# Performance work log

Hardware: AMD Instinct MI355X
Metric: run time of the kernel (lower is better)

The kernel has to match this reference:

```python
import jax, jax.numpy as jnp
import numpy as np

LEAK = 0.01  # F.leaky_relu default negative_slope


def projection(p, cam, res):
    # Weak-perspective projection to normalized [-1,1] image coords.
    # cam = [s, tx, ty]; p [B,N,3] -> [B,N,2]
    s = cam[:, 0][:, None, None]
    t = cam[:, None, 1:3]
    return s * (p[..., :2] + t)


def grid_sample_points(im_feat, pts):
    # Bilinear grid_sample with align_corners=True, zeros padding,
    # specialized to a [B,N,1,2] point grid (matches points.unsqueeze(2)).
    # im_feat [B,C,H,W], pts [B,N,2] in [-1,1] -> [B,C,N]
    B, C, H, W = im_feat.shape
    N = pts.shape[1]
    x = (pts[..., 0] + 1.0) * 0.5 * (W - 1)
    y = (pts[..., 1] + 1.0) * 0.5 * (H - 1)
    x0 = jnp.floor(x)
    y0 = jnp.floor(y)
    x1 = x0 + 1.0
    y1 = y0 + 1.0
    wx1 = x - x0
    wx0 = 1.0 - wx1
    wy1 = y - y0
    wy0 = 1.0 - wy1
    feat_flat = im_feat.reshape(B, C, H * W)

    def gather(xi, yi, w):
        valid = (xi >= 0) & (xi <= W - 1) & (yi >= 0) & (yi <= H - 1)
        xc = jnp.clip(xi, 0, W - 1).astype(jnp.int32)
        yc = jnp.clip(yi, 0, H - 1).astype(jnp.int32)
        idx = (yc * W + xc)[:, None, :]  # [B,1,N]
        g = jnp.take_along_axis(feat_flat, jnp.broadcast_to(idx, (B, C, N)), axis=2)
        return g * (w * valid.astype(w.dtype))[:, None, :]

    return (gather(x0, y0, wx0 * wy0) + gather(x1, y0, wx1 * wy0)
            + gather(x0, y1, wx0 * wy1) + gather(x1, y1, wx1 * wy1))


def reduce_dim(feat, W0, b0, W1, b1, W2, b2):
    # feat [B,C0,N]; Conv1d kernel_size=1 == channel matmul.
    def conv1x1(x, W, b):
        return jnp.einsum('oc,bcn->bon', W, x) + b[None, :, None]

    y = jax.nn.leaky_relu(conv1x1(feat, W0, b0), LEAK)
    y = jax.nn.leaky_relu(conv1x1(jnp.concatenate([y, feat], axis=1), W1, b1), LEAK)
    y = conv1x1(jnp.concatenate([y, feat], axis=1), W2, b2)
    y = jax.nn.relu(y)  # last_op
    return y.reshape(y.shape[0], -1)  # [B, C_p*N]


def setup_inputs() -> dict:
    key = jax.random.key(0)
    ks = jax.random.split(key, 9)
    B, N, C, H, Wd = 64, 431, 256, 56, 56
    dims = [256, 128, 64, 5]
    p = jax.random.normal(ks[0], (B, N, 3), jnp.float32)
    cam = jax.random.uniform(ks[1], (B, 3), jnp.float32)
    s_feat = jax.random.normal(ks[2], (B, C, H, Wd), jnp.float32)
    W0 = jax.random.normal(ks[3], (dims[1], dims[0]), jnp.float32) * 0.02
    b0 = jnp.zeros((dims[1],), jnp.float32)
    W1 = jax.random.normal(ks[4], (dims[2], dims[1] + dims[0]), jnp.float32) * 0.02
    b1 = jnp.zeros((dims[2],), jnp.float32)
    W2 = jax.random.normal(ks[5], (dims[3], dims[2] + dims[0]), jnp.float32) * 0.02
    b2 = jnp.zeros((dims[3],), jnp.float32)
    return {"p": p, "cam": cam, "s_feat": s_feat,
            "W0": W0, "b0": b0, "W1": W1, "b1": b1, "W2": W2, "b2": b2,
            "res": 224}


def reference(p, cam, s_feat, W0, b0, W1, b1, W2, b2, res):
    p2d = projection(p, cam, res)                 # [B,N,2]
    point_feat = grid_sample_points(s_feat, p2d)  # [B,C_s,N]
    return reduce_dim(point_feat, W0, b0, W1, b1, W2, b2)  # [B, C_p*N]
```

## Files before the change

### kernel.cpp

```cpp
#include <hip/hip_runtime.h>


#define B_   64
#define N_   431
#define C_   256
#define H_   56
#define W_   56
#define HW_  3136
#define PPB  16
#define NT_  27
#define NPAD (NT_ * PPB)

#define Y0S  136
#define Y1S  72

typedef __attribute__((ext_vector_type(8))) short short8;
typedef __attribute__((ext_vector_type(4))) float f32x4;

__device__ __forceinline__ ushort f2bf(float f) {
    unsigned u = __float_as_uint(f);
    u += 0x7fffu + ((u >> 16) & 1u);
    return (ushort)(u >> 16);
}
__device__ __forceinline__ uint pack2(float lo, float hi) {
    return (uint)f2bf(lo) | ((uint)f2bf(hi) << 16);
}
__device__ __forceinline__ float lo16(uint u) { return __uint_as_float(u << 16); }
__device__ __forceinline__ float hi16(uint u) { return __uint_as_float(u & 0xffff0000u); }

#define WTOT (128 * 256 + 64 * 384 + 16 * 320)
#define GB_  (B_ * 64)

__global__ __launch_bounds__(256, 6) void gather_kernel(
    const float* __restrict__ p,
    const float* __restrict__ cam,
    const float* __restrict__ sfeat,
    const float* __restrict__ W0,
    const float* __restrict__ W1,
    const float* __restrict__ W2,
    ushort* __restrict__ feat,
    ushort* __restrict__ W0b,
    ushort* __restrict__ W1b,
    ushort* __restrict__ W2p)
{
    const int bx = blockIdx.x;
    if (bx >= GB_) {
        const int t0 = (bx - GB_) * 256 + threadIdx.x;
        for (int i = t0; i < WTOT; i += 8 * 256) {
            if (i < 128 * 256) {
                W0b[i] = f2bf(W0[i]);
            } else if (i < 128 * 256 + 64 * 384) {
                const int j = i - 128 * 256;
                W1b[j] = f2bf(W1[j]);
            } else {
                const int j = i - (128 * 256 + 64 * 384);
                const int r = j / 320, c = j - r * 320;
                W2p[j] = (r < 5) ? f2bf(W2[r * 320 + c]) : (ushort)0;
            }
        }
        return;
    }

    __shared__ uint plane01[HW_];
    __shared__ uint plane23[HW_];

    const int b  = bx >> 6;
    const int cg = bx & 63;
    const int c0 = cg * 4;
    const int t  = threadIdx.x;

    {
        const float4* __restrict__ s0 = (const float4*)(sfeat + ((size_t)b * C_ + c0 + 0) * HW_);
        const float4* __restrict__ s1 = (const float4*)(sfeat + ((size_t)b * C_ + c0 + 1) * HW_);
        const float4* __restrict__ s2 = (const float4*)(sfeat + ((size_t)b * C_ + c0 + 2) * HW_);
        const float4* __restrict__ s3 = (const float4*)(sfeat + ((size_t)b * C_ + c0 + 3) * HW_);
        for (int k = t; k < HW_ / 4; k += 256) {
            const float4 a = s0[k], bb = s1[k];
            uint4 u01;
            u01.x = pack2(a.x, bb.x); u01.y = pack2(a.y, bb.y);
            u01.z = pack2(a.z, bb.z); u01.w = pack2(a.w, bb.w);
            *(uint4*)&plane01[k * 4] = u01;
            const float4 c = s2[k], d = s3[k];
            uint4 u23;
            u23.x = pack2(c.x, d.x); u23.y = pack2(c.y, d.y);
            u23.z = pack2(c.z, d.z); u23.w = pack2(c.w, d.w);
            *(uint4*)&plane23[k * 4] = u23;
        }
    }
    __syncthreads();

    const float s  = cam[b * 3 + 0];
    const float tx = cam[b * 3 + 1];
    const float ty = cam[b * 3 + 2];
    ushort* __restrict__ fdst = feat + ((size_t)b * 64 + cg) * NPAD * 4;

    for (int n = t; n < NPAD; n += 256) {
        int   i00 = 0, i10 = 0, i01 = 0, i11 = 0;
        float w00 = 0.f, w10 = 0.f, w01 = 0.f, w11 = 0.f;
        if (n < N_) {
            const float px = p[((size_t)b * N_ + n) * 3 + 0];
            const float py = p[((size_t)b * N_ + n) * 3 + 1];
            const float x = (s * (px + tx) + 1.f) * 0.5f * (float)(W_ - 1);
            const float y = (s * (py + ty) + 1.f) * 0.5f * (float)(H_ - 1);
            const float x0f = floorf(x), y0f = floorf(y);
            const float wx1 = x - x0f, wx0 = 1.f - wx1;
            const float wy1 = y - y0f, wy0 = 1.f - wy1;
            const int ix0 = (int)x0f, iy0 = (int)y0f;
            const int ix1 = ix0 + 1,  iy1 = iy0 + 1;
            const bool vx0 = (ix0 >= 0) & (ix0 <= W_ - 1);
            const bool vx1 = (ix1 >= 0) & (ix1 <= W_ - 1);
            const bool vy0 = (iy0 >= 0) & (iy0 <= H_ - 1);
            const bool vy1 = (iy1 >= 0) & (iy1 <= H_ - 1);
            const int cx0 = min(max(ix0, 0), W_ - 1);
            const int cx1 = min(max(ix1, 0), W_ - 1);
            const int cy0 = min(max(iy0, 0), H_ - 1);
            const int cy1 = min(max(iy1, 0), H_ - 1);
            w00 = (vx0 & vy0) ? wx0 * wy0 : 0.f;
            w10 = (vx1 & vy0) ? wx1 * wy0 : 0.f;
            w01 = (vx0 & vy1) ? wx0 * wy1 : 0.f;
            w11 = (vx1 & vy1) ? wx1 * wy1 : 0.f;
            i00 = cy0 * W_ + cx0;  i10 = cy0 * W_ + cx1;
            i01 = cy1 * W_ + cx0;  i11 = cy1 * W_ + cx1;
        }
        const uint a00 = plane01[i00], a10 = plane01[i10], a01 = plane01[i01], a11 = plane01[i11];
        const uint c00 = plane23[i00], c10 = plane23[i10], c01 = plane23[i01], c11 = plane23[i11];
        const float v0 = w00 * lo16(a00) + w10 * lo16(a10) + w01 * lo16(a01) + w11 * lo16(a11);
        const float v1 = w00 * hi16(a00) + w10 * hi16(a10) + w01 * hi16(a01) + w11 * hi16(a11);
        const float v2 = w00 * lo16(c00) + w10 * lo16(c10) + w01 * lo16(c01) + w11 * lo16(c11);
        const float v3 = w00 * hi16(c00) + w10 * hi16(c10) + w01 * hi16(c01) + w11 * hi16(c11);
        ushort4 r;
        r.x = f2bf(v0); r.y = f2bf(v1); r.z = f2bf(v2); r.w = f2bf(v3);
        *(ushort4*)(fdst + (size_t)n * 4) = r;
    }
}

__global__ __launch_bounds__(256, 4) void mlp_kernel(
    const ushort* __restrict__ feat,
    const ushort* __restrict__ W0b,
    const float* __restrict__ b0,
    const ushort* __restrict__ W1b,
    const float* __restrict__ b1,
    const ushort* __restrict__ W2p,
    const float* __restrict__ b2,
    float* __restrict__ out)
{
    __shared__ ushort y0_s[PPB * Y0S];
    __shared__ ushort y1_s[PPB * Y1S];

    const int tid  = threadIdx.x;
    const int w    = tid >> 6;
    const int l    = tid & 63;
    const int m    = l & 15;
    const int q    = l >> 4;
    const int tile = blockIdx.x;
    const int b    = blockIdx.y;
    const int n0   = tile * PPB;
    const int n    = n0 + m;

    const ushort* __restrict__ fb = feat + (size_t)b * 64 * NPAD * 4;
    short8 af[8];
    #pragma unroll
    for (int ks = 0; ks < 8; ++ks) {
        const int cg0 = 8 * ks + 2 * q;
        union { short8 v; uint2 u[2]; } tmp;
        tmp.u[0] = *(const uint2*)(fb + ((size_t)cg0 * NPAD + n) * 4);
        tmp.u[1] = *(const uint2*)(fb + ((size_t)(cg0 + 1) * NPAD + n) * 4);
        af[ks] = tmp.v;
    }

    {
        f32x4 acc0 = {0.f, 0.f, 0.f, 0.f};
        f32x4 acc1 = {0.f, 0.f, 0.f, 0.f};
        const ushort* __restrict__ wr0 = W0b + ((size_t)(2 * w) * 16 + m) * 256 + 8 * q;
        const ushort* __restrict__ wr1 = wr0 + 16 * 256;
        #pragma unroll
        for (int ks = 0; ks < 8; ++ks) {
            const short8 w0 = *(const short8*)(wr0 + 32 * ks);
            const short8 w1 = *(const short8*)(wr1 + 32 * ks);
            acc0 = __builtin_amdgcn_mfma_f32_16x16x32_bf16(af[ks], w0, acc0, 0, 0, 0);
            acc1 = __builtin_amdgcn_mfma_f32_16x16x32_bf16(af[ks], w1, acc1, 0, 0, 0);
        }
        const int o0 = (2 * w) * 16 + m, o1 = o0 + 16;
        const float bias0 = b0[o0], bias1 = b0[o1];
        #pragma unroll
        for (int r = 0; r < 4; ++r) {
            float v0 = acc0[r] + bias0; v0 = (v0 > 0.f) ? v0 : 0.01f * v0;
            float v1 = acc1[r] + bias1; v1 = (v1 > 0.f) ? v1 : 0.01f * v1;
            y0_s[(q * 4 + r) * Y0S + o0] = f2bf(v0);
            y0_s[(q * 4 + r) * Y0S + o1] = f2bf(v1);
        }
    }
    __syncthreads();

    {
        f32x4 acc = {0.f, 0.f, 0.f, 0.f};
        const ushort* __restrict__ wr = W1b + ((size_t)w * 16 + m) * 384 + 8 * q;
        #pragma unroll
        for (int ks = 0; ks < 4; ++ks) {
            const short8 a  = *(const short8*)(y0_s + m * Y0S + 32 * ks + 8 * q);
            const short8 bb = *(const short8*)(wr + 32 * ks);
            acc = __builtin_amdgcn_mfma_f32_16x16x32_bf16(a, bb, acc, 0, 0, 0);
        }
        #pragma unroll
        for (int ks = 4; ks < 12; ++ks) {
            const short8 bb = *(const short8*)(wr + 32 * ks);
            acc = __builtin_amdgcn_mfma_f32_16x16x32_bf16(af[ks - 4], bb, acc, 0, 0, 0);
        }
        const int o = w * 16 + m;
        const float bias = b1[o];
        #pragma unroll
        for (int r = 0; r < 4; ++r) {
            float v = acc[r] + bias; v = (v > 0.f) ? v : 0.01f * v;
            y1_s[(q * 4 + r) * Y1S + o] = f2bf(v);
        }
    }
    __syncthreads();

    if (w == 0) {
        f32x4 acc = {0.f, 0.f, 0.f, 0.f};
        const ushort* __restrict__ wr = W2p + (size_t)m * 320 + 8 * q;
        #pragma unroll
        for (int ks = 0; ks < 2; ++ks) {
            const short8 a  = *(const short8*)(y1_s + m * Y1S + 32 * ks + 8 * q);
            const short8 bb = *(const short8*)(wr + 32 * ks);
            acc = __builtin_amdgcn_mfma_f32_16x16x32_bf16(a, bb, acc, 0, 0, 0);
        }
        #pragma unroll
        for (int ks = 2; ks < 10; ++ks) {
            const short8 bb = *(const short8*)(wr + 32 * ks);
            acc = __builtin_amdgcn_mfma_f32_16x16x32_bf16(af[ks - 2], bb, acc, 0, 0, 0);
        }
        if (m < 5) {
            const float bias = b2[m];
            #pragma unroll
            for (int r = 0; r < 4; ++r) {
                const int nn = n0 + q * 4 + r;
                if (nn < N_) {
                    float v = acc[r] + bias;
                    out[((size_t)b * 5 + m) * N_ + nn] = (v > 0.f) ? v : 0.f;
                }
            }
        }
    }
}

__global__ __launch_bounds__(256, 4) void maf_fallback_kernel(
    const float* __restrict__ p, const float* __restrict__ cam,
    const float* __restrict__ sfeat,
    const float* __restrict__ W0, const float* __restrict__ b0,
    const float* __restrict__ W1, const float* __restrict__ b1,
    const float* __restrict__ W2, const float* __restrict__ b2,
    float* __restrict__ out)
{
    __shared__ float feat_s[PPB][C_ + 4];
    __shared__ float y0_s[PPB][128 + 4];
    __shared__ float y1_s[PPB][64 + 4];

    const int tid = threadIdx.x;
    const int b   = blockIdx.y;
    const int n0  = blockIdx.x * PPB;
    const float s  = cam[b * 3 + 0];
    const float tx = cam[b * 3 + 1];
    const float ty = cam[b * 3 + 2];
    {
        const int c = tid;
        const float* __restrict__ fb = sfeat + ((size_t)b * C_ + c) * HW_;
        for (int pp = 0; pp < PPB; ++pp) {
            const int n = n0 + pp;
            float val = 0.f;
            if (n < N_) {
                const float px = p[((size_t)b * N_ + n) * 3 + 0];
                const float py = p[((size_t)b * N_ + n) * 3 + 1];
                const float x = (s * (px + tx) + 1.f) * 0.5f * (float)(W_ - 1);
                const float y = (s * (py + ty) + 1.f) * 0.5f * (float)(H_ - 1);
                const float x0f = floorf(x), y0f = floorf(y);
                const float wx1 = x - x0f, wx0 = 1.f - wx1;
                const float wy1 = y - y0f, wy0 = 1.f - wy1;
                const int ix0 = (int)x0f, iy0 = (int)y0f;
                const int ix1 = ix0 + 1,  iy1 = iy0 + 1;
                const bool vx0 = (ix0 >= 0) & (ix0 <= W_ - 1);
                const bool vx1 = (ix1 >= 0) & (ix1 <= W_ - 1);
                const bool vy0 = (iy0 >= 0) & (iy0 <= H_ - 1);
                const bool vy1 = (iy1 >= 0) & (iy1 <= H_ - 1);
                const int cx0 = min(max(ix0, 0), W_ - 1);
                const int cx1 = min(max(ix1, 0), W_ - 1);
                const int cy0 = min(max(iy0, 0), H_ - 1);
                const int cy1 = min(max(iy1, 0), H_ - 1);
                const float w00 = (vx0 & vy0) ? wx0 * wy0 : 0.f;
                const float w10 = (vx1 & vy0) ? wx1 * wy0 : 0.f;
                const float w01 = (vx0 & vy1) ? wx0 * wy1 : 0.f;
                const float w11 = (vx1 & vy1) ? wx1 * wy1 : 0.f;
                val = w00 * fb[cy0 * W_ + cx0] + w10 * fb[cy0 * W_ + cx1]
                    + w01 * fb[cy1 * W_ + cx0] + w11 * fb[cy1 * W_ + cx1];
            }
            feat_s[pp][c] = val;
        }
    }
    __syncthreads();
    {
        const int o = tid & 127, pg = tid >> 7, p0 = pg * 8;
        const float* __restrict__ wr = W0 + (size_t)o * 256;
        float acc[8] = {0, 0, 0, 0, 0, 0, 0, 0};
        for (int k = 0; k < 256; k += 4) {
            const float4 w = *(const float4*)(wr + k);
            for (int i = 0; i < 8; ++i) {
                const float4 f = *(const float4*)&feat_s[p0 + i][k];
                acc[i] += w.x * f.x + w.y * f.y + w.z * f.z + w.w * f.w;
            }
        }
        const float bias = b0[o];
        for (int i = 0; i < 8; ++i) {
            const float v = acc[i] + bias;
            y0_s[p0 + i][o] = (v > 0.f) ? v : 0.01f * v;
        }
    }
    __syncthreads();
    {
        const int o = tid & 63, pg = tid >> 6, p0 = pg * 4;
        const float* __restrict__ wr = W1 + (size_t)o * 384;
        float acc[4] = {0, 0, 0, 0};
        for (int k = 0; k < 128; k += 4) {
            const float4 w = *(const float4*)(wr + k);
            for (int i = 0; i < 4; ++i) {
                const float4 f = *(const float4*)&y0_s[p0 + i][k];
                acc[i] += w.x * f.x + w.y * f.y + w.z * f.z + w.w * f.w;
            }
        }
        for (int k = 0; k < 256; k += 4) {
            const float4 w = *(const float4*)(wr + 128 + k);
            for (int i = 0; i < 4; ++i) {
                const float4 f = *(const float4*)&feat_s[p0 + i][k];
                acc[i] += w.x * f.x + w.y * f.y + w.z * f.z + w.w * f.w;
            }
        }
        const float bias = b1[o];
        for (int i = 0; i < 4; ++i) {
            const float v = acc[i] + bias;
            y1_s[p0 + i][o] = (v > 0.f) ? v : 0.01f * v;
        }
    }
    __syncthreads();
    if (tid < 80) {
        const int o = tid >> 4, pp = tid & 15;
        const float* __restrict__ wr = W2 + (size_t)o * 320;
        float acc = 0.f;
        for (int k = 0; k < 64; k += 4) {
            const float4 w = *(const float4*)(wr + k);
            const float4 f = *(const float4*)&y1_s[pp][k];
            acc += w.x * f.x + w.y * f.y + w.z * f.z + w.w * f.w;
        }
        for (int k = 0; k < 256; k += 4) {
            const float4 w = *(const float4*)(wr + 64 + k);
            const float4 f = *(const float4*)&feat_s[pp][k];
            acc += w.x * f.x + w.y * f.y + w.z * f.z + w.w * f.w;
        }
        const int n = n0 + pp;
        if (n < N_) {
            float v = acc + b2[o];
            out[((size_t)b * 5 + o) * N_ + n] = (v > 0.f) ? v : 0.f;
        }
    }
}

extern "C" void kernel_launch(void* const* d_in, const int* in_sizes, int n_in,
                              void* d_out, int out_size, void* d_ws, size_t ws_size,
                              hipStream_t stream) {
    const float* p     = (const float*)d_in[0];
    const float* cam   = (const float*)d_in[1];
    const float* sfeat = (const float*)d_in[2];
    const float* W0    = (const float*)d_in[3];
    const float* b0    = (const float*)d_in[4];
    const float* W1    = (const float*)d_in[5];
    const float* b1    = (const float*)d_in[6];
    const float* W2    = (const float*)d_in[7];
    const float* b2    = (const float*)d_in[8];
    float* out = (float*)d_out;

    const size_t feat_elems = (size_t)B_ * 64 * NPAD * 4;
    size_t off = feat_elems;
    const size_t w0_off = off; off += 128 * 256;
    const size_t w1_off = off; off += 64 * 384;
    const size_t w2_off = off; off += 16 * 320;
    const size_t need = off * sizeof(ushort);

    if (ws_size >= need) {
        ushort* feat = (ushort*)d_ws;
        ushort* W0b  = feat + w0_off;
        ushort* W1b  = feat + w1_off;
        ushort* W2p  = feat + w2_off;
        gather_kernel<<<GB_ + 8, 256, 0, stream>>>(
            p, cam, sfeat, W0, W1, W2, feat, W0b, W1b, W2p);
        mlp_kernel<<<dim3(NT_, B_), 256, 0, stream>>>(
            feat, W0b, b0, W1b, b1, W2p, b2, out);
    } else {
        maf_fallback_kernel<<<dim3(NT_, B_), 256, 0, stream>>>(
            p, cam, sfeat, W0, b0, W1, b1, W2, b2, out);
    }
}
```

Baseline: 336.7 us.

## Replace two-kernel bf16 gather+MFMA pipeline with single fused fp32 kernel

Drops the separate gather kernel, which streamed every full feature plane into LDS as bf16, and the MFMA-based MLP kernel. A single fused kernel replaces them. It first computes the bilinear indices and weights for the block's 16 points into shared memory. Each thread then gathers one channel directly from global memory, and the three 1x1 convs run in fp32 scalar FMA from LDS. This avoids reading the whole feature map and the intermediate workspace round trip, but the gathers are now scattered across channel planes (uncoalesced) and the matmuls lose tensor-core use.

After: 519.9 us. +54.4%, slower.

```diff
diff --git a/kernel.cpp b/kernel.cpp
--- a/kernel.cpp
+++ b/kernel.cpp
@@ -9,95 +9,34 @@
 #define HW_  3136
 #define PPB  16
 #define NT_  27
-#define NPAD (NT_ * PPB)
 
-#define Y0S  136
-#define Y1S  72
-
-typedef __attribute__((ext_vector_type(8))) short short8;
-typedef __attribute__((ext_vector_type(4))) float f32x4;
-
-__device__ __forceinline__ ushort f2bf(float f) {
-    unsigned u = __float_as_uint(f);
-    u += 0x7fffu + ((u >> 16) & 1u);
-    return (ushort)(u >> 16);
-}
-__device__ __forceinline__ uint pack2(float lo, float hi) {
-    return (uint)f2bf(lo) | ((uint)f2bf(hi) << 16);
-}
-__device__ __forceinline__ float lo16(uint u) { return __uint_as_float(u << 16); }
-__device__ __forceinline__ float hi16(uint u) { return __uint_as_float(u & 0xffff0000u); }
-
-#define WTOT (128 * 256 + 64 * 384 + 16 * 320)
-#define GB_  (B_ * 64)
-
-__global__ __launch_bounds__(256, 6) void gather_kernel(
+__global__ __launch_bounds__(256, 4) void maf_fused_kernel(
     const float* __restrict__ p,
     const float* __restrict__ cam,
     const float* __restrict__ sfeat,
-    const float* __restrict__ W0,
-    const float* __restrict__ W1,
-    const float* __restrict__ W2,
-    ushort* __restrict__ feat,
-    ushort* __restrict__ W0b,
-    ushort* __restrict__ W1b,
-    ushort* __restrict__ W2p)
+    const float* __restrict__ W0, const float* __restrict__ b0,
+    const float* __restrict__ W1, const float* __restrict__ b1,
+    const float* __restrict__ W2, const float* __restrict__ b2,
+    float* __restrict__ out)
 {
-    const int bx = blockIdx.x;
-    if (bx >= GB_) {
-        const int t0 = (bx - GB_) * 256 + threadIdx.x;
-        for (int i = t0; i < WTOT; i += 8 * 256) {
-            if (i < 128 * 256) {
-                W0b[i] = f2bf(W0[i]);
-            } else if (i < 128 * 256 + 64 * 384) {
-                const int j = i - 128 * 256;
-                W1b[j] = f2bf(W1[j]);
-            } else {
-                const int j = i - (128 * 256 + 64 * 384);
-                const int r = j / 320, c = j - r * 320;
-                W2p[j] = (r < 5) ? f2bf(W2[r * 320 + c]) : (ushort)0;
-            }
-        }
-        return;
-    }
+    __shared__ float feat_s[PPB][C_ + 4];
+    __shared__ float y0_s[PPB][128 + 4];
+    __shared__ float y1_s[PPB][64 + 4];
+    __shared__ int   gi_s[PPB][4];
+    __shared__ float gw_s[PPB][4];
 
-    __shared__ uint plane01[HW_];
-    __shared__ uint plane23[HW_];
+    const int tid = threadIdx.x;
+    const int b   = blockIdx.y;
+    const int n0  = blockIdx.x * PPB;
 
-    const int b  = bx >> 6;
-    const int cg = bx & 63;
-    const int c0 = cg * 4;
-    const int t  = threadIdx.x;
-
-    {
-        const float4* __restrict__ s0 = (const float4*)(sfeat + ((size_t)b * C_ + c0 + 0) * HW_);
-        const float4* __restrict__ s1 = (const float4*)(sfeat + ((size_t)b * C_ + c0 + 1) * HW_);
-        const float4* __restrict__ s2 = (const float4*)(sfeat + ((size_t)b * C_ + c0 + 2) * HW_);
-        const float4* __restrict__ s3 = (const float4*)(sfeat + ((size_t)b * C_ + c0 + 3) * HW_);
-        for (int k = t; k < HW_ / 4; k += 256) {
-            const float4 a = s0[k], bb = s1[k];
-            uint4 u01;
-            u01.x = pack2(a.x, bb.x); u01.y = pack2(a.y, bb.y);
-            u01.z = pack2(a.z, bb.z); u01.w = pack2(a.w, bb.w);
-            *(uint4*)&plane01[k * 4] = u01;
-            const float4 c = s2[k], d = s3[k];
-            uint4 u23;
-            u23.x = pack2(c.x, d.x); u23.y = pack2(c.y, d.y);
-            u23.z = pack2(c.z, d.z); u23.w = pack2(c.w, d.w);
-            *(uint4*)&plane23[k * 4] = u23;
-        }
-    }
-    __syncthreads();
-
-    const float s  = cam[b * 3 + 0];
-    const float tx = cam[b * 3 + 1];
-    const float ty = cam[b * 3 + 2];
-    ushort* __restrict__ fdst = feat + ((size_t)b * 64 + cg) * NPAD * 4;
-
-    for (int n = t; n < NPAD; n += 256) {
+    if (tid < PPB) {
+        const int n = n0 + tid;
         int   i00 = 0, i10 = 0, i01 = 0, i11 = 0;
         float w00 = 0.f, w10 = 0.f, w01 = 0.f, w11 = 0.f;
         if (n < N_) {
+            const float s  = cam[b * 3 + 0];
+            const float tx = cam[b * 3 + 1];
+            const float ty = cam[b * 3 + 2];
             const float px = p[((size_t)b * N_ + n) * 3 + 0];
             const float py = p[((size_t)b * N_ + n) * 3 + 1];
             const float x = (s * (px + tx) + 1.f) * 0.5f * (float)(W_ - 1);
@@ -122,205 +61,55 @@
             i00 = cy0 * W_ + cx0;  i10 = cy0 * W_ + cx1;
             i01 = cy1 * W_ + cx0;  i11 = cy1 * W_ + cx1;
         }
-        const uint a00 = plane01[i00], a10 = plane01[i10], a01 = plane01[i01], a11 = plane01[i11];
-        const uint c00 = plane23[i00], c10 = plane23[i10], c01 = plane23[i01], c11 = plane23[i11];
-        const float v0 = w00 * lo16(a00) + w10 * lo16(a10) + w01 * lo16(a01) + w11 * lo16(a11);
-        const float v1 = w00 * hi16(a00) + w10 * hi16(a10) + w01 * hi16(a01) + w11 * hi16(a11);
-        const float v2 = w00 * lo16(c00) + w10 * lo16(c10) + w01 * lo16(c01) + w11 * lo16(c11);
-        const float v3 = w00 * hi16(c00) + w10 * hi16(c10) + w01 * hi16(c01) + w11 * hi16(c11);
-        ushort4 r;
-        r.x = f2bf(v0); r.y = f2bf(v1); r.z = f2bf(v2); r.w = f2bf(v3);
-        *(ushort4*)(fdst + (size_t)n * 4) = r;
+        gi_s[tid][0] = i00; gi_s[tid][1] = i10;
+        gi_s[tid][2] = i01; gi_s[tid][3] = i11;
+        gw_s[tid][0] = w00; gw_s[tid][1] = w10;
+        gw_s[tid][2] = w01; gw_s[tid][3] = w11;
     }
-}
-
-__global__ __launch_bounds__(256, 4) void mlp_kernel(
-    const ushort* __restrict__ feat,
-    const ushort* __restrict__ W0b,
-    const float* __restrict__ b0,
-    const ushort* __restrict__ W1b,
-    const float* __restrict__ b1,
-    const ushort* __restrict__ W2p,
-    const float* __restrict__ b2,
-    float* __restrict__ out)
-{
-    __shared__ ushort y0_s[PPB * Y0S];
-    __shared__ ushort y1_s[PPB * Y1S];
-
-    const int tid  = threadIdx.x;
-    const int w    = tid >> 6;
-    const int l    = tid & 63;
-    const int m    = l & 15;
-    const int q    = l >> 4;
-    const int tile = blockIdx.x;
-    const int b    = blockIdx.y;
-    const int n0   = tile * PPB;
-    const int n    = n0 + m;
-
-    const ushort* __restrict__ fb = feat + (size_t)b * 64 * NPAD * 4;
-    short8 af[8];
-    #pragma unroll
-    for (int ks = 0; ks < 8; ++ks) {
-        const int cg0 = 8 * ks + 2 * q;
-        union { short8 v; uint2 u[2]; } tmp;
-        tmp.u[0] = *(const uint2*)(fb + ((size_t)cg0 * NPAD + n) * 4);
-        tmp.u[1] = *(const uint2*)(fb + ((size_t)(cg0 + 1) * NPAD + n) * 4);
-        af[ks] = tmp.v;
-    }
+    __syncthreads();
 
     {
-        f32x4 acc0 = {0.f, 0.f, 0.f, 0.f};
-        f32x4 acc1 = {0.f, 0.f, 0.f, 0.f};
-        const ushort* __restrict__ wr0 = W0b + ((size_t)(2 * w) * 16 + m) * 256 + 8 * q;
-        const ushort* __restrict__ wr1 = wr0 + 16 * 256;
-        #pragma unroll
-        for (int ks = 0; ks < 8; ++ks) {
-            const short8 w0 = *(const short8*)(wr0 + 32 * ks);
-            const short8 w1 = *(const short8*)(wr1 + 32 * ks);
-            acc0 = __builtin_amdgcn_mfma_f32_16x16x32_bf16(af[ks], w0, acc0, 0, 0, 0);
-            acc1 = __builtin_amdgcn_mfma_f32_16x16x32_bf16(af[ks], w1, acc1, 0, 0, 0);
-        }
-        const int o0 = (2 * w) * 16 + m, o1 = o0 + 16;
-        const float bias0 = b0[o0], bias1 = b0[o1];
-        #pragma unroll
-        for (int r = 0; r < 4; ++r) {
-            float v0 = acc0[r] + bias0; v0 = (v0 > 0.f) ? v0 : 0.01f * v0;
-            float v1 = acc1[r] + bias1; v1 = (v1 > 0.f) ? v1 : 0.01f * v1;
-            y0_s[(q * 4 + r) * Y0S + o0] = f2bf(v0);
-            y0_s[(q * 4 + r) * Y0S + o1] = f2bf(v1);
+        const float* __restrict__ fb = sfeat + ((size_t)b * C_ + tid) * HW_;
+        #pragma unroll 4
+        for (int pp = 0; pp < PPB; ++pp) {
+            const int   i0 = gi_s[pp][0], i1 = gi_s[pp][1];
+            const int   i2 = gi_s[pp][2], i3 = gi_s[pp][3];
+            const float w0 = gw_s[pp][0], w1 = gw_s[pp][1];
+            const float w2 = gw_s[pp][2], w3 = gw_s[pp][3];
+            feat_s[pp][tid] = w0 * fb[i0] + w1 * fb[i1]
+                            + w2 * fb[i2] + w3 * fb[i3];
         }
     }
     __syncthreads();
 
-    {
-        f32x4 acc = {0.f, 0.f, 0.f, 0.f};
-        const ushort* __restrict__ wr = W1b + ((size_t)w * 16 + m) * 384 + 8 * q;
-        #pragma unroll
-        for (int ks = 0; ks < 4; ++ks) {
-            const short8 a  = *(const short8*)(y0_s + m * Y0S + 32 * ks + 8 * q);
-            const short8 bb = *(const short8*)(wr + 32 * ks);
-            acc = __builtin_amdgcn_mfma_f32_16x16x32_bf16(a, bb, acc, 0, 0, 0);
-        }
-        #pragma unroll
-        for (int ks = 4; ks < 12; ++ks) {
-            const short8 bb = *(const short8*)(wr + 32 * ks);
-            acc = __builtin_amdgcn_mfma_f32_16x16x32_bf16(af[ks - 4], bb, acc, 0, 0, 0);
-        }
-        const int o = w * 16 + m;
-        const float bias = b1[o];
-        #pragma unroll
-        for (int r = 0; r < 4; ++r) {
-            float v = acc[r] + bias; v = (v > 0.f) ? v : 0.01f * v;
-            y1_s[(q * 4 + r) * Y1S + o] = f2bf(v);
-        }
-    }
-    __syncthreads();
-
-    if (w == 0) {
-        f32x4 acc = {0.f, 0.f, 0.f, 0.f};
-        const ushort* __restrict__ wr = W2p + (size_t)m * 320 + 8 * q;
-        #pragma unroll
-        for (int ks = 0; ks < 2; ++ks) {
-            const short8 a  = *(const short8*)(y1_s + m * Y1S + 32 * ks + 8 * q);
-            const short8 bb = *(const short8*)(wr + 32 * ks);
-            acc = __builtin_amdgcn_mfma_f32_16x16x32_bf16(a, bb, acc, 0, 0, 0);
-        }
-        #pragma unroll
-        for (int ks = 2; ks < 10; ++ks) {
-            const short8 bb = *(const short8*)(wr + 32 * ks);
-            acc = __builtin_amdgcn_mfma_f32_16x16x32_bf16(af[ks - 2], bb, acc, 0, 0, 0);
-        }
-        if (m < 5) {
-            const float bias = b2[m];
-            #pragma unroll
-            for (int r = 0; r < 4; ++r) {
-                const int nn = n0 + q * 4 + r;
-                if (nn < N_) {
-                    float v = acc[r] + bias;
-                    out[((size_t)b * 5 + m) * N_ + nn] = (v > 0.f) ? v : 0.f;
-                }
-            }
-        }
-    }
-}
-
-__global__ __launch_bounds__(256, 4) void maf_fallback_kernel(
-    const float* __restrict__ p, const float* __restrict__ cam,
-    const float* __restrict__ sfeat,
-    const float* __restrict__ W0, const float* __restrict__ b0,
-    const float* __restrict__ W1, const float* __restrict__ b1,
-    const float* __restrict__ W2, const float* __restrict__ b2,
-    float* __restrict__ out)
-{
-    __shared__ float feat_s[PPB][C_ + 4];
-    __shared__ float y0_s[PPB][128 + 4];
-    __shared__ float y1_s[PPB][64 + 4];
-
-    const int tid = threadIdx.x;
-    const int b   = blockIdx.y;
-    const int n0  = blockIdx.x * PPB;
-    const float s  = cam[b * 3 + 0];
-    const float tx = cam[b * 3 + 1];
-    const float ty = cam[b * 3 + 2];
-    {
-        const int c = tid;
-        const float* __restrict__ fb = sfeat + ((size_t)b * C_ + c) * HW_;
-        for (int pp = 0; pp < PPB; ++pp) {
-            const int n = n0 + pp;
-            float val = 0.f;
-            if (n < N_) {
-                const float px = p[((size_t)b * N_ + n) * 3 + 0];
-                const float py = p[((size_t)b * N_ + n) * 3 + 1];
-                const float x = (s * (px + tx) + 1.f) * 0.5f * (float)(W_ - 1);
-                const float y = (s * (py + ty) + 1.f) * 0.5f * (float)(H_ - 1);
-                const float x0f = floorf(x), y0f = floorf(y);
-                const float wx1 = x - x0f, wx0 = 1.f - wx1;
-                const float wy1 = y - y0f, wy0 = 1.f - wy1;
-                const int ix0 = (int)x0f, iy0 = (int)y0f;
-                const int ix1 = ix0 + 1,  iy1 = iy0 + 1;
-                const bool vx0 = (ix0 >= 0) & (ix0 <= W_ - 1);
-                const bool vx1 = (ix1 >= 0) & (ix1 <= W_ - 1);
-                const bool vy0 = (iy0 >= 0) & (iy0 <= H_ - 1);
-                const bool vy1 = (iy1 >= 0) & (iy1 <= H_ - 1);
-                const int cx0 = min(max(ix0, 0), W_ - 1);
-                const int cx1 = min(max(ix1, 0), W_ - 1);
-                const int cy0 = min(max(iy0, 0), H_ - 1);
-                const int cy1 = min(max(iy1, 0), H_ - 1);
-                const float w00 = (vx0 & vy0) ? wx0 * wy0 : 0.f;
-                const float w10 = (vx1 & vy0) ? wx1 * wy0 : 0.f;
-                const float w01 = (vx0 & vy1) ? wx0 * wy1 : 0.f;
-                const float w11 = (vx1 & vy1) ? wx1 * wy1 : 0.f;
-                val = w00 * fb[cy0 * W_ + cx0] + w10 * fb[cy0 * W_ + cx1]
-                    + w01 * fb[cy1 * W_ + cx0] + w11 * fb[cy1 * W_ + cx1];
-            }
-            feat_s[pp][c] = val;
-        }
-    }
-    __syncthreads();
     {
         const int o = tid & 127, pg = tid >> 7, p0 = pg * 8;
         const float* __restrict__ wr = W0 + (size_t)o * 256;
         float acc[8] = {0, 0, 0, 0, 0, 0, 0, 0};
         for (int k = 0; k < 256; k += 4) {
             const float4 w = *(const float4*)(wr + k);
+            #pragma unroll
             for (int i = 0; i < 8; ++i) {
                 const float4 f = *(const float4*)&feat_s[p0 + i][k];
                 acc[i] += w.x * f.x + w.y * f.y + w.z * f.z + w.w * f.w;
             }
         }
         const float bias = b0[o];
+        #pragma unroll
         for (int i = 0; i < 8; ++i) {
             const float v = acc[i] + bias;
             y0_s[p0 + i][o] = (v > 0.f) ? v : 0.01f * v;
         }
     }
     __syncthreads();
+
     {
         const int o = tid & 63, pg = tid >> 6, p0 = pg * 4;
         const float* __restrict__ wr = W1 + (size_t)o * 384;
         float acc[4] = {0, 0, 0, 0};
         for (int k = 0; k < 128; k += 4) {
             const float4 w = *(const float4*)(wr + k);
+            #pragma unroll
             for (int i = 0; i < 4; ++i) {
                 const float4 f = *(const float4*)&y0_s[p0 + i][k];
                 acc[i] += w.x * f.x + w.y * f.y + w.z * f.z + w.w * f.w;
@@ -328,18 +117,21 @@
         }
         for (int k = 0; k < 256; k += 4) {
             const float4 w = *(const float4*)(wr + 128 + k);
+            #pragma unroll
             for (int i = 0; i < 4; ++i) {
                 const float4 f = *(const float4*)&feat_s[p0 + i][k];
                 acc[i] += w.x * f.x + w.y * f.y + w.z * f.z + w.w * f.w;
             }
         }
         const float bias = b1[o];
+        #pragma unroll
         for (int i = 0; i < 4; ++i) {
             const float v = acc[i] + bias;
             y1_s[p0 + i][o] = (v > 0.f) ? v : 0.01f * v;
         }
     }
     __syncthreads();
+
     if (tid < 80) {
         const int o = tid >> 4, pp = tid & 15;
         const float* __restrict__ wr = W2 + (size_t)o * 320;
@@ -356,7 +148,7 @@
         }
         const int n = n0 + pp;
         if (n < N_) {
-            float v = acc + b2[o];
+            const float v = acc + b2[o];
             out[((size_t)b * 5 + o) * N_ + n] = (v > 0.f) ? v : 0.f;
         }
     }
@@ -376,24 +168,8 @@
     const float* b2    = (const float*)d_in[8];
     float* out = (float*)d_out;
 
-    const size_t feat_elems = (size_t)B_ * 64 * NPAD * 4;
-    size_t off = feat_elems;
-    const size_t w0_off = off; off += 128 * 256;
-    const size_t w1_off = off; off += 64 * 384;
-    const size_t w2_off = off; off += 16 * 320;
-    const size_t need = off * sizeof(ushort);
+    (void)d_ws; (void)ws_size;
 
-    if (ws_size >= need) {
-        ushort* feat = (ushort*)d_ws;
-        ushort* W0b  = feat + w0_off;
-        ushort* W1b  = feat + w1_off;
-        ushort* W2p  = feat + w2_off;
-        gather_kernel<<<GB_ + 8, 256, 0, stream>>>(
-            p, cam, sfeat, W0, W1, W2, feat, W0b, W1b, W2p);
-        mlp_kernel<<<dim3(NT_, B_), 256, 0, stream>>>(
-            feat, W0b, b0, W1b, b1, W2p, b2, out);
-    } else {
-        maf_fallback_kernel<<<dim3(NT_, B_), 256, 0, stream>>>(
-            p, cam, sfeat, W0, b0, W1, b1, W2, b2, out);
-    }
+    maf_fused_kernel<<<dim3(NT_, B_), 256, 0, stream>>>(
+        p, cam, sfeat, W0, b0, W1, b1, W2, b2, out);
 }
```
